# Optimization experiments

Hardware: AMD Instinct MI355X
Metric: run time of the kernel (lower is better)

The kernel has to match this reference:

```python
import jax, jax.numpy as jnp
import numpy as np

N_NODES = 50000
N_EDGES = 800000
IN_DIM = 256
HID = 256
NUM_LAYERS = 2


def _sage(xin, src, dst, inv_deg, W_l, b_l, W_r):
    # PyG SAGEConv (mean aggr): lin_l(mean of src features scattered to dst) + lin_r(x)
    agg = jax.ops.segment_sum(xin[src], dst, num_segments=xin.shape[0]) * inv_deg
    return agg @ W_l + b_l + xin @ W_r


def _mgdsgu(x, src, dst, inv_deg, h, Wx_l, bx_l, Wx_r, Wh_l, bh_l, Wh_r, Wb1, bb1, Wb2, bb2):
    # hid->hid conv order: 0=sage_hidden, 1=sage_single_h, 2=sage_update_h, 3=sage_candidate_h
    # in ->hid conv order: 0=sage_single_x, 1=sage_update_x, 2=sage_candidate_x
    h_N = _sage(h, src, dst, inv_deg, Wh_l[0], bh_l[0], Wh_r[0])
    # predict_missing_info: r = zeros so r_v = beta; gamma is computed in the
    # original but multiplied by zero -> no effect (omitted).
    beta = jnp.tanh(h @ Wb1 + bb1 + h_N @ Wb2 + bb2)
    m = h + beta - h_N
    h_N = h_N + m  # == h + beta, kept as written for clarity
    r = jax.nn.sigmoid(_sage(x, src, dst, inv_deg, Wx_l[0], bx_l[0], Wx_r[0])
                       + _sage(h_N, src, dst, inv_deg, Wh_l[1], bh_l[1], Wh_r[1]))
    z = jax.nn.sigmoid(_sage(x, src, dst, inv_deg, Wx_l[1], bx_l[1], Wx_r[1])
                       + _sage(h_N, src, dst, inv_deg, Wh_l[2], bh_l[2], Wh_r[2]))
    h_tilde = jnp.tanh(_sage(x, src, dst, inv_deg, Wx_l[2], bx_l[2], Wx_r[2])
                       + _sage(r * h_N, src, dst, inv_deg, Wh_l[3], bh_l[3], Wh_r[3]))
    return (1.0 - z) * h_N + z * h_tilde


def setup_inputs() -> dict:
    key = jax.random.key(0)
    ks = jax.random.split(key, 12)
    sx = 1.0 / np.sqrt(IN_DIM)
    sh = 1.0 / np.sqrt(HID)
    inp = {
        "x": jax.random.normal(ks[0], (N_NODES, IN_DIM), dtype=jnp.float32),
        "edge_index": jax.random.randint(ks[1], (2, N_EDGES), 0, N_NODES, dtype=jnp.int64),
        "Wx_l": jax.random.normal(ks[2], (3, IN_DIM, HID), dtype=jnp.float32) * sx,
        "bx_l": jnp.zeros((3, HID), dtype=jnp.float32),
        "Wx_r": jax.random.normal(ks[3], (3, IN_DIM, HID), dtype=jnp.float32) * sx,
        "Wh_l": jax.random.normal(ks[4], (4, HID, HID), dtype=jnp.float32) * sh,
        "bh_l": jnp.zeros((4, HID), dtype=jnp.float32),
        "Wh_r": jax.random.normal(ks[5], (4, HID, HID), dtype=jnp.float32) * sh,
        "Wb1": jax.random.normal(ks[6], (HID, HID), dtype=jnp.float32) * sh,
        "bb1": jnp.zeros((HID,), dtype=jnp.float32),
        "Wb2": jax.random.normal(ks[7], (HID, HID), dtype=jnp.float32) * sh,
        "bb2": jnp.zeros((HID,), dtype=jnp.float32),
        "We1": jax.random.normal(ks[8], (2 * HID, HID), dtype=jnp.float32) * (1.0 / np.sqrt(2 * HID)),
        "be1": jnp.zeros((HID,), dtype=jnp.float32),
        "We2": jax.random.normal(ks[9], (HID, 1), dtype=jnp.float32) * sh,
        "be2": jnp.zeros((1,), dtype=jnp.float32),
    }
    return inp


def reference(x, edge_index, Wx_l, bx_l, Wx_r, Wh_l, bh_l, Wh_r,
              Wb1, bb1, Wb2, bb2, We1, be1, We2, be2):
    src, dst = edge_index[0], edge_index[1]
    deg = jax.ops.segment_sum(jnp.ones((src.shape[0],), dtype=x.dtype), dst,
                              num_segments=x.shape[0])
    inv_deg = (1.0 / jnp.maximum(deg, 1.0))[:, None]  # [N, 1]

    h = jnp.zeros((x.shape[0], HID), dtype=x.dtype)
    for _ in range(NUM_LAYERS):
        h = _mgdsgu(x, src, dst, inv_deg, h, Wx_l, bx_l, Wx_r,
                    Wh_l, bh_l, Wh_r, Wb1, bb1, Wb2, bb2)

    # edge embeddings: concat(src emb, dst emb) -> MLP -> sigmoid
    edge_emb = jnp.concatenate([h[src], h[dst]], axis=1)  # [E, 2H]
    hidden = jax.nn.relu(edge_emb @ We1 + be1)
    preds = jax.nn.sigmoid(hidden @ We2 + be2)  # [E, 1]
    return (preds, h)
```

## Files before the change

kernel.cpp:

```cpp
#include <hip/hip_runtime.h>
#include <math.h>

#define HID 256
#define LROW 40

typedef __bf16 bf16x8 __attribute__((ext_vector_type(8)));
typedef float  f32x4  __attribute__((ext_vector_type(4)));
typedef unsigned short us8 __attribute__((ext_vector_type(8)));

__device__ __forceinline__ float sigmoidf_(float x){ return 1.0f/(1.0f + __expf(-x)); }
__device__ __forceinline__ unsigned short f2b(float f){
  __bf16 b = (__bf16)f; return __builtin_bit_cast(unsigned short, b);
}
__device__ __forceinline__ float b2f(unsigned short u){
  return (float)__builtin_bit_cast(__bf16, u);
}

__device__ __forceinline__ int edge_src(const int* ei, int e, int is64){
  return is64 ? ei[2*e] : ei[e];
}
__device__ __forceinline__ int edge_dst(const int* ei, int e, int E, int is64){
  return is64 ? ei[2*(E+e)] : ei[E+e];
}

__global__ void detect_kernel(const int* __restrict__ ei, int* __restrict__ flag){
  __shared__ int any;
  if (threadIdx.x == 0) any = 0;
  __syncthreads();
  if (ei[2*threadIdx.x + 1] != 0) atomicOr(&any, 1);
  __syncthreads();
  if (threadIdx.x == 0) *flag = any ? 0 : 1;
}

__global__ void count_kernel(const int* __restrict__ ei, const int* __restrict__ flag,
                             int* __restrict__ deg_i, int E){
  int e = blockIdx.x*blockDim.x + threadIdx.x;
  if (e >= E) return;
  int is64 = *flag;
  atomicAdd(&deg_i[edge_dst(ei,e,E,is64)], 1);
}

__global__ __launch_bounds__(1024) void scan_kernel(const int* __restrict__ deg_i,
  int* __restrict__ row_ptr, float* __restrict__ inv_deg, int N)
{
  __shared__ int wsum[16];
  __shared__ int carry_s;
  int tid = threadIdx.x, lane = tid & 63, wid = tid >> 6;
  if (tid == 0) carry_s = 0;
  __syncthreads();
  for (int base = 0; base < N; base += 1024){
    int i = base + tid;
    int v = (i < N) ? deg_i[i] : 0;
    int s = v;
    #pragma unroll
    for (int off = 1; off < 64; off <<= 1){
      int t = __shfl_up(s, off, 64);
      if (lane >= off) s += t;
    }
    if (lane == 63) wsum[wid] = s;
    __syncthreads();
    if (tid == 0){
      int run = 0;
      for (int w2 = 0; w2 < 16; ++w2){ int t = wsum[w2]; wsum[w2] = run; run += t; }
    }
    __syncthreads();
    int excl = carry_s + wsum[wid] + s - v;
    if (i < N){
      row_ptr[i] = excl;
      inv_deg[i] = 1.0f / fmaxf((float)v, 1.0f);
    }
    __syncthreads();
    if (tid == 1023) carry_s = excl + v;
    __syncthreads();
  }
  if (threadIdx.x == 0) row_ptr[N] = carry_s;
}

__global__ void fill_kernel(const int* __restrict__ ei, const int* __restrict__ flag,
                            const int* __restrict__ row_ptr, int* __restrict__ cursor,
                            int* __restrict__ col_src, int E){
  int e = blockIdx.x*blockDim.x + threadIdx.x;
  if (e >= E) return;
  int is64 = *flag;
  int d = edge_dst(ei,e,E,is64);
  int pos = atomicAdd(&cursor[d], 1);
  col_src[row_ptr[d] + pos] = edge_src(ei,e,is64);
}

__global__ __launch_bounds__(256) void conv_kernel(const float* __restrict__ in,
                                                   unsigned short* __restrict__ out, int n4){
  int i = blockIdx.x*256 + threadIdx.x;
  if (i >= n4) return;
  float4 v = *(const float4*)&in[(size_t)i*4];
  ushort4 o; o.x=f2b(v.x); o.y=f2b(v.y); o.z=f2b(v.z); o.w=f2b(v.w);
  *(ushort4*)&out[(size_t)i*4] = o;
}

__global__ __launch_bounds__(256) void wconv_kernel(
  const float* __restrict__ Wx_l, const float* __restrict__ Wx_r,
  const float* __restrict__ Wh_l, const float* __restrict__ Wh_r,
  const float* __restrict__ Wb1,  const float* __restrict__ Wb2,
  const float* __restrict__ We1,  unsigned short* __restrict__ Wt)
{
  int widx = blockIdx.x;
  int n = blockIdx.y;
  int k = threadIdx.x;
  const float* src;
  if      (widx < 3)  src = Wx_l + widx*65536;
  else if (widx < 6)  src = Wx_r + (widx-3)*65536;
  else if (widx < 10) src = Wh_l + (widx-6)*65536;
  else if (widx < 14) src = Wh_r + (widx-10)*65536;
  else if (widx == 14) src = Wb1;
  else if (widx == 15) src = Wb2;
  else                src = We1 + (widx-16)*65536;
  Wt[(size_t)widx*65536 + n*256 + k] = f2b(src[k*256 + n]);
}

__global__ __launch_bounds__(256) void comp_kernel(
  const float* __restrict__ A, const float* __restrict__ B,
  const float* __restrict__ add, unsigned short* __restrict__ dst)
{
  __shared__ float col[256];
  int n = blockIdx.x, k = threadIdx.x;
  col[k] = B[k*256 + n];
  __syncthreads();
  float s = add ? add[k*256 + n] : 0.f;
  #pragma unroll 8
  for (int j = 0; j < 256; ++j) s = fmaf(A[k*256 + j], col[j], s);
  dst[n*256 + k] = f2b(s);
}

__global__ __launch_bounds__(256) void aggregate_b_kernel(
    const unsigned short* __restrict__ X, unsigned short* __restrict__ out,
    const int* __restrict__ row_ptr, const int* __restrict__ col_src,
    const float* __restrict__ inv_deg, int N)
{
  int v = blockIdx.x*4 + (threadIdx.x >> 6);
  int lane = threadIdx.x & 63;
  if (v >= N) return;
  int beg = row_ptr[v], end = row_ptr[v+1];
  float a0=0.f, a1=0.f, a2=0.f, a3=0.f;
  int e = beg;
  for (; e + 8 <= end; e += 8){
    int sidx[8];
    #pragma unroll
    for (int t = 0; t < 8; ++t) sidx[t] = col_src[e + t];
    #pragma unroll
    for (int t = 0; t < 8; ++t){
      ushort4 u = *(const ushort4*)&X[(size_t)sidx[t]*HID + lane*4];
      a0 += b2f(u.x); a1 += b2f(u.y); a2 += b2f(u.z); a3 += b2f(u.w);
    }
  }
  for (; e < end; ++e){
    int s0 = col_src[e];
    ushort4 u = *(const ushort4*)&X[(size_t)s0*HID + lane*4];
    a0 += b2f(u.x); a1 += b2f(u.y); a2 += b2f(u.z); a3 += b2f(u.w);
  }
  float w = inv_deg[v];
  ushort4 o; o.x=f2b(a0*w); o.y=f2b(a1*w); o.z=f2b(a2*w); o.w=f2b(a3*w);
  *(ushort4*)&out[(size_t)v*HID + lane*4] = o;
}

__global__ __launch_bounds__(256) void rowprep_kernel(
  const float* __restrict__ bh_l, const float* __restrict__ bb1, const float* __restrict__ bb2,
  const float* __restrict__ Wb2, const float* __restrict__ Wh_l, const float* __restrict__ Wh_r,
  float* __restrict__ brow, float* __restrict__ hrow,
  float* __restrict__ rowL1, float* __restrict__ rowR1,
  float* __restrict__ rowL2, float* __restrict__ rowR2)
{
  __shared__ float sh[256];
  __shared__ float sh2[256];
  int j = threadIdx.x;
  sh[j] = bh_l[j];
  __syncthreads();
  float acc = bb1[j] + bb2[j];
  for (int k = 0; k < 256; ++k) acc = fmaf(sh[k], Wb2[k*256 + j], acc);
  float hr = tanhf(acc);
  brow[j] = acc;
  hrow[j] = hr; sh2[j] = hr;
  __syncthreads();
  const float* Whl1 = Wh_l + 65536;  const float* Whr1 = Wh_r + 65536;
  const float* Whl2 = Wh_l + 131072; const float* Whr2 = Wh_r + 131072;
  float a1=0.f, b1=0.f, a2=0.f, b2v=0.f;
  for (int k = 0; k < 256; ++k){
    float hv = sh2[k];
    a1  = fmaf(hv, Whl1[k*256+j], a1);
    b1  = fmaf(hv, Whr1[k*256+j], b1);
    a2  = fmaf(hv, Whl2[k*256+j], a2);
    b2v = fmaf(hv, Whr2[k*256+j], b2v);
  }
  rowL1[j] = a1; rowR1[j] = b1 + bh_l[256 + j];
  rowL2[j] = a2; rowR2[j] = b2v + bh_l[512 + j];
}

struct GJob {
  const unsigned short *A0,*W0,*A1,*W1,*A2,*W2,*A3,*W3;
  const float *bias,*bias2,*Z,*HN;
  const float *rowA,*rowB,*mulrow,*mulmat;
  const int* deg;
  float* outF; unsigned short* outB;
  int hn_bcast;
};

template<int MODE>
__global__ __launch_bounds__(256) void mgemm2_kernel(GJob j0, GJob j1, int M)
{
  __shared__ unsigned short Al[128*LROW];
  __shared__ unsigned short Bl[128*LROW];
  const GJob& J = (blockIdx.y >> 1) ? j1 : j0;
  const int col0 = (blockIdx.y & 1) * 128;
  const int tid  = threadIdx.x;
  const int lane = tid & 63, w = tid >> 6;
  const int wr = w >> 1, wc = w & 1;
  const int lane15 = lane & 15, laneq = (lane >> 4) * 8;
  const int row0 = blockIdx.x * 128;

  f32x4 acc[4][4];
  #pragma unroll
  for (int m = 0; m < 4; ++m)
    #pragma unroll
    for (int n = 0; n < 4; ++n) acc[m][n] = (f32x4)0.f;

  const unsigned short* pa[4]; const unsigned short* pw[4];
  int np = 0;
  if (J.A0){ pa[np]=J.A0; pw[np]=J.W0; ++np; }
  if (J.A1){ pa[np]=J.A1; pw[np]=J.W1; ++np; }
  if (J.A2){ pa[np]=J.A2; pw[np]=J.W2; ++np; }
  if (J.A3){ pa[np]=J.A3; pw[np]=J.W3; ++np; }
  const int steps = np * 8;

  const int srow = tid >> 1;
  const int koff = (tid & 1) * 16;
  const int arow = (row0 + srow > M-1) ? (M-1) : (row0 + srow);
  const size_t abase = (size_t)arow*HID + koff;
  const size_t bbase = (size_t)(col0 + srow)*HID + koff;
  const int sidx = srow*LROW + koff;

  uint4 A0a,A0b,B0a,B0b, A1a,A1b,B1a,B1b;
  auto loadR = [&](int sp, uint4& a0, uint4& a1, uint4& b0, uint4& b1){
    const unsigned short* Ap = pa[sp >> 3];
    const unsigned short* Wp = pw[sp >> 3];
    const int k0 = (sp & 7) * 32;
    const unsigned short* ga = Ap + abase + k0;
    const unsigned short* gb = Wp + bbase + k0;
    a0 = *(const uint4*)ga;  a1 = *(const uint4*)(ga + 8);
    b0 = *(const uint4*)gb;  b1 = *(const uint4*)(gb + 8);
  };
  auto compute = [&](){
    bf16x8 af[4], bfr[4];
    #pragma unroll
    for (int m = 0; m < 4; ++m)
      af[m] = *(const bf16x8*)&Al[(wr*64 + m*16 + lane15)*LROW + laneq];
    #pragma unroll
    for (int n = 0; n < 4; ++n)
      bfr[n] = *(const bf16x8*)&Bl[(wc*64 + n*16 + lane15)*LROW + laneq];
    #pragma unroll
    for (int m = 0; m < 4; ++m)
      #pragma unroll
      for (int n = 0; n < 4; ++n)
        acc[m][n] = __builtin_amdgcn_mfma_f32_16x16x32_bf16(af[m], bfr[n], acc[m][n], 0, 0, 0);
  };

  loadR(0, A0a,A0b,B0a,B0b);
  loadR(1, A1a,A1b,B1a,B1b);
  for (int s = 0; s < steps; s += 2){
    __syncthreads();
    *(uint4*)&Al[sidx] = A0a; *(uint4*)&Al[sidx+8] = A0b;
    *(uint4*)&Bl[sidx] = B0a; *(uint4*)&Bl[sidx+8] = B0b;
    __syncthreads();
    if (s + 2 < steps) loadR(s+2, A0a,A0b,B0a,B0b);
    compute();
    __syncthreads();
    *(uint4*)&Al[sidx] = A1a; *(uint4*)&Al[sidx+8] = A1b;
    *(uint4*)&Bl[sidx] = B1a; *(uint4*)&Bl[sidx+8] = B1b;
    __syncthreads();
    if (s + 3 < steps) loadR(s+3, A1a,A1b,B1a,B1b);
    compute();
  }

  #pragma unroll
  for (int n = 0; n < 4; ++n){
    int gc = col0 + wc*64 + n*16 + lane15;
    float badd = 0.f;
    if (J.bias)  badd += J.bias[gc];
    if (J.bias2) badd += J.bias2[gc];
    float rA = 0.f, rB = 0.f, mr = 1.f, hnb = 0.f;
    if (MODE == 1){
      if (J.rowA){ rA = J.rowA[gc]; rB = J.rowB[gc]; }
      if (J.mulrow) mr = J.mulrow[gc];
    }
    if (MODE == 3 && J.hn_bcast) hnb = J.HN[gc];
    #pragma unroll
    for (int m = 0; m < 4; ++m){
      int rbse = row0 + wr*64 + m*16 + ((lane >> 4) << 2);
      #pragma unroll
      for (int r = 0; r < 4; ++r){
        int gr = rbse + r;
        if (gr >= M) continue;
        size_t idx = (size_t)gr*HID + gc;
        float p = acc[m][n][r] + badd;
        float v;
        if (MODE == 0) v = p;
        else if (MODE == 1){
          float g = (J.rowA && J.deg) ? ((J.deg[gr] > 0) ? 1.f : 0.f) : 0.f;
          v = sigmoidf_(p + g*rA + rB);
          if (J.mulrow) v *= mr;
          if (J.mulmat) v *= J.mulmat[idx];
        } else if (MODE == 2){
          v = J.HN[idx] + tanhf(p);
        } else {
          float z  = J.Z[idx];
          float hv = J.hn_bcast ? hnb : J.HN[idx];
          v = (1.f - z)*hv + z*tanhf(p);
        }
        if (J.outF) J.outF[idx] = v;
        if (J.outB) J.outB[idx] = f2b(v);
      }
    }
  }
}

__global__ __launch_bounds__(256) void edge_pred_kernel(
  const unsigned short* __restrict__ P, const unsigned short* __restrict__ Q,
  const int* __restrict__ ei, const int* __restrict__ flag,
  const float* __restrict__ We2, const float* __restrict__ be2,
  float* __restrict__ preds, int E)
{
  int wid = blockIdx.x*8 + (threadIdx.x >> 5);
  int l = threadIdx.x & 31;
  if (wid >= E) return;
  int is64 = *flag;
  int s = edge_src(ei, wid, is64);
  int d = edge_dst(ei, wid, E, is64);
  us8 p8 = *(const us8*)&P[(size_t)s*HID + l*8];
  us8 q8 = *(const us8*)&Q[(size_t)d*HID + l*8];
  float4 w0 = *(const float4*)&We2[l*8];
  float4 w1 = *(const float4*)&We2[l*8 + 4];
  float part = 0.f;
  #pragma unroll
  for (int j = 0; j < 4; ++j)
    part = fmaf(fmaxf(b2f(p8[j]) + b2f(q8[j]), 0.f), (&w0.x)[j], part);
  #pragma unroll
  for (int j = 0; j < 4; ++j)
    part = fmaf(fmaxf(b2f(p8[4+j]) + b2f(q8[4+j]), 0.f), (&w1.x)[j], part);
  #pragma unroll
  for (int off = 16; off > 0; off >>= 1) part += __shfl_down(part, off, 32);
  if (l == 0) preds[wid] = sigmoidf_(part + be2[0]);
}

typedef const unsigned short* cus;
typedef const float* cf;

template<int MODE>
static void launch_fused(const GJob& a, const GJob* b, int M, hipStream_t s){
  dim3 g((M + 127)/128, b ? 4 : 2), blk(256);
  mgemm2_kernel<MODE><<<g, blk, 0, s>>>(a, b ? *b : a, M);
}

extern "C" void kernel_launch(void* const* d_in, const int* in_sizes, int n_in,
                              void* d_out, int out_size, void* d_ws, size_t ws_size,
                              hipStream_t stream)
{
  const float* x    = (const float*)d_in[0];
  const int*   ei   = (const int*)  d_in[1];
  const float* Wx_l = (const float*)d_in[2];
  const float* bx_l = (const float*)d_in[3];
  const float* Wx_r = (const float*)d_in[4];
  const float* Wh_l = (const float*)d_in[5];
  const float* bh_l = (const float*)d_in[6];
  const float* Wh_r = (const float*)d_in[7];
  const float* Wb1  = (const float*)d_in[8];
  const float* bb1  = (const float*)d_in[9];
  const float* Wb2  = (const float*)d_in[10];
  const float* bb2  = (const float*)d_in[11];
  const float* We1  = (const float*)d_in[12];
  const float* be1  = (const float*)d_in[13];
  const float* We2  = (const float*)d_in[14];
  const float* be2  = (const float*)d_in[15];

  const int N = in_sizes[0] / HID;
  const int E = in_sizes[1] / 2;
  cf NUL = nullptr; cus NUB = nullptr; const int* NULI = nullptr;

  size_t off = 0;
  auto alloc = [&](size_t bytes) -> void* {
    void* p = (char*)d_ws + off;
    off += (bytes + 255) & ~(size_t)255;
    return p;
  };
  int*   deg_i   = (int*)  alloc((size_t)N*4);
  int*   cursor  = (int*)  alloc((size_t)N*4);
  int*   row_ptr = (int*)  alloc(((size_t)N+1)*4);
  int*   col_src = (int*)  alloc((size_t)E*4);
  float* inv_deg = (float*)alloc((size_t)N*4);
  int*   flag    = (int*)  alloc(256);
  float* brow    = (float*)alloc(1024);
  float* hrow    = (float*)alloc(1024);
  float* rowL1   = (float*)alloc(1024);
  float* rowR1   = (float*)alloc(1024);
  float* rowL2   = (float*)alloc(1024);
  float* rowR2   = (float*)alloc(1024);
  unsigned short* Wt = (unsigned short*)alloc((size_t)18*65536*2);
  float* F0 = (float*)alloc((size_t)N*HID*4);
  float* F1 = (float*)alloc((size_t)N*HID*4);
  unsigned short* b0 = (unsigned short*)alloc((size_t)N*HID*2);
  unsigned short* b1 = (unsigned short*)alloc((size_t)N*HID*2);
  unsigned short* b2 = (unsigned short*)alloc((size_t)N*HID*2);
  unsigned short* b3 = (unsigned short*)alloc((size_t)N*HID*2);
  unsigned short* b4 = (unsigned short*)alloc((size_t)N*HID*2);

  float* preds = (float*)d_out;
  float* H     = preds + E;

  auto WT = [&](int i) -> cus { return Wt + (size_t)i*65536; };
  const float* bx0 = bx_l;  const float* bx1 = bx_l + 256; const float* bx2 = bx_l + 512;
  const float* bh1 = bh_l + 256;
  const float* bh2 = bh_l + 512; const float* bh3 = bh_l + 768;

  const int eb  = (E + 255)/256;
  const int nb4 = (N + 3)/4;
  const int n4b = (N*64 + 255)/256;

  auto mkjob = [&](cus A0,cus W0,cus A1,cus W1,cus A2,cus W2,cus A3,cus W3,
                   cf bias, cf bias2, cf Z, cf HN, int hnb,
                   cf rA, cf rB, cf mr, cf mm, const int* dg,
                   float* oF, unsigned short* oB) -> GJob {
    GJob g;
    g.A0=A0; g.W0=W0; g.A1=A1; g.W1=W1; g.A2=A2; g.W2=W2; g.A3=A3; g.W3=W3;
    g.bias=bias; g.bias2=bias2; g.Z=Z; g.HN=HN; g.hn_bcast=hnb;
    g.rowA=rA; g.rowB=rB; g.mulrow=mr; g.mulmat=mm; g.deg=dg;
    g.outF=oF; g.outB=oB;
    return g;
  };

  hipMemsetAsync(deg_i, 0, (size_t)N*4, stream);
  hipMemsetAsync(cursor, 0, (size_t)N*4, stream);
  detect_kernel<<<1,256,0,stream>>>(ei, flag);
  count_kernel<<<eb,256,0,stream>>>(ei, flag, deg_i, E);
  scan_kernel<<<1,1024,0,stream>>>(deg_i, row_ptr, inv_deg, N);
  fill_kernel<<<eb,256,0,stream>>>(ei, flag, row_ptr, cursor, col_src, E);

  conv_kernel<<<n4b,256,0,stream>>>(x, b0, N*64);
  wconv_kernel<<<dim3(18,256),256,0,stream>>>(Wx_l, Wx_r, Wh_l, Wh_r, Wb1, Wb2, We1, Wt);
  comp_kernel<<<256,256,0,stream>>>(Wh_l, Wb2, nullptr, (unsigned short*)WT(14));
  comp_kernel<<<256,256,0,stream>>>(Wh_r, Wb2, Wb1,     (unsigned short*)WT(15));
  rowprep_kernel<<<1,256,0,stream>>>(bh_l, bb1, bb2, Wb2, Wh_l, Wh_r,
                                     brow, hrow, rowL1, rowR1, rowL2, rowR2);

  aggregate_b_kernel<<<nb4,256,0,stream>>>(b0, b1, row_ptr, col_src, inv_deg, N);
  {
    GJob jt = mkjob(b1,WT(0), b0,WT(3), NUB,NUB, NUB,NUB, bx0,NUL, NUL,NUL,0,
                    rowL1,rowR1, hrow,NUL, deg_i, nullptr, b2);
    GJob jz = mkjob(b1,WT(1), b0,WT(4), NUB,NUB, NUB,NUB, bx1,NUL, NUL,NUL,0,
                    rowL2,rowR2, NUL,NUL, deg_i, F0, nullptr);
    launch_fused<1>(jt, &jz, N, stream);
  }
  aggregate_b_kernel<<<nb4,256,0,stream>>>(b2, b3, row_ptr, col_src, inv_deg, N);
  {
    GJob jh = mkjob(b3,WT(9), b2,WT(13), b1,WT(2), b0,WT(5), bx2,bh3, F0,hrow,1,
                    NUL,NUL, NUL,NUL, NULI, F0, b4);
    launch_fused<3>(jh, nullptr, N, stream);
  }

  aggregate_b_kernel<<<nb4,256,0,stream>>>(b4, b2, row_ptr, col_src, inv_deg, N);
  {
    GJob jn = mkjob(b2,WT(14), b4,WT(15), NUB,NUB, NUB,NUB, brow,NUL, NUL,F0,0,
                    NUL,NUL, NUL,NUL, NULI, F1, b3);
    launch_fused<2>(jn, nullptr, N, stream);
  }
  aggregate_b_kernel<<<nb4,256,0,stream>>>(b3, b2, row_ptr, col_src, inv_deg, N);
  {
    GJob jt = mkjob(b2,WT(7), b3,WT(11), b1,WT(0), b0,WT(3), bx0,bh1, NUL,NUL,0,
                    NUL,NUL, NUL,F1, NULI, nullptr, b4);
    GJob jz = mkjob(b2,WT(8), b3,WT(12), b1,WT(1), b0,WT(4), bx1,bh2, NUL,NUL,0,
                    NUL,NUL, NUL,NUL, NULI, F0, nullptr);
    launch_fused<1>(jt, &jz, N, stream);
  }
  aggregate_b_kernel<<<nb4,256,0,stream>>>(b4, b2, row_ptr, col_src, inv_deg, N);
  {
    GJob jh = mkjob(b2,WT(9), b4,WT(13), b1,WT(2), b0,WT(5), bx2,bh3, F0,F1,0,
                    NUL,NUL, NUL,NUL, NULI, H, b3);
    launch_fused<3>(jh, nullptr, N, stream);
  }

  {
    GJob jp = mkjob(b3,WT(16), NUB,NUB, NUB,NUB, NUB,NUB, be1,NUL, NUL,NUL,0,
                    NUL,NUL, NUL,NUL, NULI, nullptr, b2);
    GJob jq = mkjob(b3,WT(17), NUB,NUB, NUB,NUB, NUB,NUB, NUL,NUL, NUL,NUL,0,
                    NUL,NUL, NUL,NUL, NULI, nullptr, b4);
    launch_fused<0>(jp, &jq, N, stream);
  }
  edge_pred_kernel<<<(E+7)/8,256,0,stream>>>(b2, b4, ei, flag, We2, be2, preds, E);
}
```

Before: 1.307 ms.

## Widen GEMM tile to full 256 output columns with 512-thread blocks

The fused MFMA GEMM now computes a 128x256 output tile per block using 8 waves (2x4), instead of two 128x128 blocks per row tile. Each A tile is loaded from global memory once rather than twice, which halves A traffic and the number of blocks. The cost is a larger shared-memory footprint (W tile 256 rows) and more threads per block, so occupancy may drop and there are fewer blocks to spread across CUs.

```diff
diff --git a/kernel.cpp b/kernel.cpp
--- a/kernel.cpp
+++ b/kernel.cpp
@@ -203,15 +203,14 @@
 };
 
 template<int MODE>
-__global__ __launch_bounds__(256) void mgemm2_kernel(GJob j0, GJob j1, int M)
+__global__ __launch_bounds__(512) void mgemm3_kernel(GJob j0, GJob j1, int M)
 {
   __shared__ unsigned short Al[128*LROW];
-  __shared__ unsigned short Bl[128*LROW];
-  const GJob& J = (blockIdx.y >> 1) ? j1 : j0;
-  const int col0 = (blockIdx.y & 1) * 128;
+  __shared__ unsigned short Wl[256*LROW];
+  const GJob& J = blockIdx.y ? j1 : j0;
   const int tid  = threadIdx.x;
   const int lane = tid & 63, w = tid >> 6;
-  const int wr = w >> 1, wc = w & 1;
+  const int wr = w >> 2, wc = w & 3;
   const int lane15 = lane & 15, laneq = (lane >> 4) * 8;
   const int row0 = blockIdx.x * 128;
 
@@ -229,22 +228,24 @@
   if (J.A3){ pa[np]=J.A3; pw[np]=J.W3; ++np; }
   const int steps = np * 8;
 
-  const int srow = tid >> 1;
-  const int koff = (tid & 1) * 16;
-  const int arow = (row0 + srow > M-1) ? (M-1) : (row0 + srow);
-  const size_t abase = (size_t)arow*HID + koff;
-  const size_t bbase = (size_t)(col0 + srow)*HID + koff;
-  const int sidx = srow*LROW + koff;
-
-  uint4 A0a,A0b,B0a,B0b, A1a,A1b,B1a,B1b;
-  auto loadR = [&](int sp, uint4& a0, uint4& a1, uint4& b0, uint4& b1){
+  const int strow = tid >> 2;
+  const int koff  = (tid & 3) * 8;
+  const int garow = (row0 + strow > M-1) ? (M-1) : (row0 + strow);
+  const size_t abase  = (size_t)garow*HID + koff;
+  const size_t wbase0 = (size_t)strow*HID + koff;
+  const size_t wbase1 = (size_t)(strow + 128)*HID + koff;
+  const int asidx  = strow*LROW + koff;
+  const int wsidx0 = strow*LROW + koff;
+  const int wsidx1 = (strow + 128)*LROW + koff;
+
+  uint4 Ar0,Wr0a,Wr0b, Ar1,Wr1a,Wr1b;
+  auto loadR = [&](int sp, uint4& a, uint4& wa, uint4& wb){
     const unsigned short* Ap = pa[sp >> 3];
     const unsigned short* Wp = pw[sp >> 3];
     const int k0 = (sp & 7) * 32;
-    const unsigned short* ga = Ap + abase + k0;
-    const unsigned short* gb = Wp + bbase + k0;
-    a0 = *(const uint4*)ga;  a1 = *(const uint4*)(ga + 8);
-    b0 = *(const uint4*)gb;  b1 = *(const uint4*)(gb + 8);
+    a  = *(const uint4*)(Ap + abase  + k0);
+    wa = *(const uint4*)(Wp + wbase0 + k0);
+    wb = *(const uint4*)(Wp + wbase1 + k0);
   };
   auto compute = [&](){
     bf16x8 af[4], bfr[4];
@@ -253,7 +254,7 @@
       af[m] = *(const bf16x8*)&Al[(wr*64 + m*16 + lane15)*LROW + laneq];
     #pragma unroll
     for (int n = 0; n < 4; ++n)
-      bfr[n] = *(const bf16x8*)&Bl[(wc*64 + n*16 + lane15)*LROW + laneq];
+      bfr[n] = *(const bf16x8*)&Wl[(wc*64 + n*16 + lane15)*LROW + laneq];
     #pragma unroll
     for (int m = 0; m < 4; ++m)
       #pragma unroll
@@ -261,26 +262,28 @@
         acc[m][n] = __builtin_amdgcn_mfma_f32_16x16x32_bf16(af[m], bfr[n], acc[m][n], 0, 0, 0);
   };
 
-  loadR(0, A0a,A0b,B0a,B0b);
-  loadR(1, A1a,A1b,B1a,B1b);
+  loadR(0, Ar0,Wr0a,Wr0b);
+  loadR(1, Ar1,Wr1a,Wr1b);
   for (int s = 0; s < steps; s += 2){
     __syncthreads();
-    *(uint4*)&Al[sidx] = A0a; *(uint4*)&Al[sidx+8] = A0b;
-    *(uint4*)&Bl[sidx] = B0a; *(uint4*)&Bl[sidx+8] = B0b;
-    __syncthreads();
-    if (s + 2 < steps) loadR(s+2, A0a,A0b,B0a,B0b);
+    *(uint4*)&Al[asidx]  = Ar0;
+    *(uint4*)&Wl[wsidx0] = Wr0a;
+    *(uint4*)&Wl[wsidx1] = Wr0b;
+    __syncthreads();
+    if (s + 2 < steps) loadR(s+2, Ar0,Wr0a,Wr0b);
     compute();
     __syncthreads();
-    *(uint4*)&Al[sidx] = A1a; *(uint4*)&Al[sidx+8] = A1b;
-    *(uint4*)&Bl[sidx] = B1a; *(uint4*)&Bl[sidx+8] = B1b;
-    __syncthreads();
-    if (s + 3 < steps) loadR(s+3, A1a,A1b,B1a,B1b);
+    *(uint4*)&Al[asidx]  = Ar1;
+    *(uint4*)&Wl[wsidx0] = Wr1a;
+    *(uint4*)&Wl[wsidx1] = Wr1b;
+    __syncthreads();
+    if (s + 3 < steps) loadR(s+3, Ar1,Wr1a,Wr1b);
     compute();
   }
 
   #pragma unroll
   for (int n = 0; n < 4; ++n){
-    int gc = col0 + wc*64 + n*16 + lane15;
+    int gc = wc*64 + n*16 + lane15;
     float badd = 0.f;
     if (J.bias)  badd += J.bias[gc];
     if (J.bias2) badd += J.bias2[gc];
@@ -352,9 +355,9 @@
 typedef const float* cf;
 
 template<int MODE>
-static void launch_fused(const GJob& a, const GJob* b, int M, hipStream_t s){
-  dim3 g((M + 127)/128, b ? 4 : 2), blk(256);
-  mgemm2_kernel<MODE><<<g, blk, 0, s>>>(a, b ? *b : a, M);
+static void launch_f(const GJob& a, const GJob* b, int M, hipStream_t s){
+  dim3 g((M + 127)/128, b ? 2 : 1), blk(512);
+  mgemm3_kernel<MODE><<<g, blk, 0, s>>>(a, b ? *b : a, M);
 }
 
 extern "C" void kernel_launch(void* const* d_in, const int* in_sizes, int n_in,
@@ -453,20 +456,20 @@
                     rowL1,rowR1, hrow,NUL, deg_i, nullptr, b2);
     GJob jz = mkjob(b1,WT(1), b0,WT(4), NUB,NUB, NUB,NUB, bx1,NUL, NUL,NUL,0,
                     rowL2,rowR2, NUL,NUL, deg_i, F0, nullptr);
-    launch_fused<1>(jt, &jz, N, stream);
+    launch_f<1>(jt, &jz, N, stream);
   }
   aggregate_b_kernel<<<nb4,256,0,stream>>>(b2, b3, row_ptr, col_src, inv_deg, N);
   {
     GJob jh = mkjob(b3,WT(9), b2,WT(13), b1,WT(2), b0,WT(5), bx2,bh3, F0,hrow,1,
                     NUL,NUL, NUL,NUL, NULI, F0, b4);
-    launch_fused<3>(jh, nullptr, N, stream);
+    launch_f<3>(jh, nullptr, N, stream);
   }
 
   aggregate_b_kernel<<<nb4,256,0,stream>>>(b4, b2, row_ptr, col_src, inv_deg, N);
   {
     GJob jn = mkjob(b2,WT(14), b4,WT(15), NUB,NUB, NUB,NUB, brow,NUL, NUL,F0,0,
                     NUL,NUL, NUL,NUL, NULI, F1, b3);
-    launch_fused<2>(jn, nullptr, N, stream);
+    launch_f<2>(jn, nullptr, N, stream);
   }
   aggregate_b_kernel<<<nb4,256,0,stream>>>(b3, b2, row_ptr, col_src, inv_deg, N);
   {
@@ -474,13 +477,13 @@
                     NUL,NUL, NUL,F1, NULI, nullptr, b4);
     GJob jz = mkjob(b2,WT(8), b3,WT(12), b1,WT(1), b0,WT(4), bx1,bh2, NUL,NUL,0,
                     NUL,NUL, NUL,NUL, NULI, F0, nullptr);
-    launch_fused<1>(jt, &jz, N, stream);
+    launch_f<1>(jt, &jz, N, stream);
   }
   aggregate_b_kernel<<<nb4,256,0,stream>>>(b4, b2, row_ptr, col_src, inv_deg, N);
   {
     GJob jh = mkjob(b2,WT(9), b4,WT(13), b1,WT(2), b0,WT(5), bx2,bh3, F0,F1,0,
                     NUL,NUL, NUL,NUL, NULI, H, b3);
-    launch_fused<3>(jh, nullptr, N, stream);
+    launch_f<3>(jh, nullptr, N, stream);
   }
 
   {
@@ -488,7 +491,7 @@
                     NUL,NUL, NUL,NUL, NULI, nullptr, b2);
     GJob jq = mkjob(b3,WT(17), NUB,NUB, NUB,NUB, NUB,NUB, NUL,NUL, NUL,NUL,0,
                     NUL,NUL, NUL,NUL, NULI, nullptr, b4);
-    launch_fused<0>(jp, &jq, N, stream);
+    launch_f<0>(jp, &jq, N, stream);
   }
   edge_pred_kernel<<<(E+7)/8,256,0,stream>>>(b2, b4, ei, flag, We2, be2, preds, E);
 }
```

Result: faster. 1.160 ms (-11.2%).
